# Kernel optimization log

Measured on AMD Instinct MI355X. Metric: run time of the kernel, lower is better.

Reference implementation:

```python
import jax, jax.numpy as jnp
import numpy as np


def setup_inputs() -> dict:
    key = jax.random.key(0)
    kx, kr, kq, kk, kv = jax.random.split(key, 5)
    B, T, N, C = 4, 8, 2048, 128
    w_scale = 1.0 / np.sqrt(C)  # keep logits in a sane range
    return {
        "x": jax.random.normal(kx, (B, T, N, C), dtype=jnp.float32),
        "residual_source": jax.random.normal(kr, (B, N, C), dtype=jnp.float32),
        "Wq": jax.random.normal(kq, (C, C), dtype=jnp.float32) * w_scale,
        "Wk": jax.random.normal(kk, (C, C), dtype=jnp.float32) * w_scale,
        "Wv": jax.random.normal(kv, (C, C), dtype=jnp.float32) * w_scale,
    }


def reference(x, residual_source, Wq, Wk, Wv):
    # x: [B, T, N, C]; residual_source: [B, M, C] (expanded along T in the
    # original via unsqueeze+expand; here we exploit broadcasting instead of
    # materializing the [B, T, M, C] copy -- same math, k/v identical per T).
    q = jnp.einsum("btnc,cd->btnd", x, Wq)               # [B, T, N, D]
    k = jnp.einsum("bmc,cd->bmd", residual_source, Wk)   # [B, M, D]
    v = jnp.einsum("bmc,cd->bmd", residual_source, Wv)   # [B, M, D]
    # Unscaled attention, exactly as in the original (no 1/sqrt(d)).
    affinities = jnp.einsum("btnd,bmd->btnm", q, k)       # [B, T, N, M]
    attn = jax.nn.softmax(affinities, axis=-1)
    residual = jnp.einsum("btnm,bmd->btnd", attn, v)      # [B, T, N, D]
    return x + residual
```

## Files before the change

kernel.cpp:

```cpp
#include <hip/hip_runtime.h>


#define Bn 4
#define Tn 8
#define Nn 2048
#define Cn 128
#define Mn 2048
#define NTILES 32
#define QROWS 128
#define NQT (Nn / QROWS)

typedef __attribute__((ext_vector_type(4))) float f32x4;
typedef __attribute__((ext_vector_type(8))) _Float16 f16x8;
typedef __attribute__((address_space(3))) unsigned char lds_uc;
typedef const __attribute__((address_space(1))) unsigned char glb_uc;

__device__ __forceinline__ unsigned short f2h(float f) {
  _Float16 h = (_Float16)f;
  return __builtin_bit_cast(unsigned short, h);
}
__device__ __forceinline__ f16x8 lds_read8(const unsigned char* base, int row,
                                           int rowBytes, int colByte) {
  int byte = row * rowBytes + (colByte ^ ((row & 7) << 4));
  return *(const f16x8*)(base + byte);
}
__device__ __forceinline__ void gld16(const void* g, void* l) {
  __builtin_amdgcn_global_load_lds((glb_uc*)g, (lds_uc*)l, 16, 0, 0);
}

__global__ __launch_bounds__(256) void proj_kv_kernel(
    const float* __restrict__ rs, const float* __restrict__ Wk,
    const float* __restrict__ Wv, unsigned short* __restrict__ k_ws,
    unsigned short* __restrict__ vt_ws) {
  __shared__ unsigned char smem[48 * 1024];
  unsigned char* rsh = smem;
  unsigned char* wt = smem + 16 * 1024;

  const int bid = blockIdx.x;
  const int b = bid >> 5;
  const int kt = bid & 31;
  const int m0 = kt << 6;
  const int tid = threadIdx.x;
  const int wv = tid >> 6, lane = tid & 63;

  {
    const float4* g = (const float4*)(rs + ((size_t)b * Mn + m0) * Cn);
#pragma unroll
    for (int i = 0; i < 8; ++i) {
      int f = tid + i * 256;
      int row = f >> 5, c4 = f & 31;
      float4 v = g[f];
      int byte = row * 256 + ((c4 * 8) ^ ((row & 7) << 4));
      *(ushort4*)(rsh + byte) =
          make_ushort4(f2h(v.x), f2h(v.y), f2h(v.z), f2h(v.w));
    }
  }

#define STAGE_WT(Wp)                                                          \
  {                                                                           \
    const float4* g = (const float4*)(Wp);                                    \
    _Pragma("unroll") for (int i = 0; i < 16; ++i) {                          \
      int f = tid + i * 256;                                                  \
      int c = f >> 5, d0 = (f & 31) * 4;                                      \
      float4 v = g[f];                                                        \
      float vv[4] = {v.x, v.y, v.z, v.w};                                     \
      _Pragma("unroll") for (int j = 0; j < 4; ++j) {                         \
        int row = d0 + j;                                                     \
        int byte = row * 256 + ((c * 2) ^ ((row & 7) << 4));                  \
        *(unsigned short*)(wt + byte) = f2h(vv[j]);                           \
      }                                                                       \
    }                                                                         \
  }

  STAGE_WT(Wk);
  __syncthreads();

  const int arow = wv * 16 + (lane & 15);
  f16x8 ah[4];
#pragma unroll
  for (int ks = 0; ks < 4; ++ks)
    ah[ks] = lds_read8(rsh, arow, 256, (lane >> 4) * 16 + ks * 64);

  f32x4 acc[8];
#pragma unroll
  for (int df = 0; df < 8; ++df) acc[df] = (f32x4)(0.0f);
#pragma unroll
  for (int ks = 0; ks < 4; ++ks)
#pragma unroll
    for (int df = 0; df < 8; ++df) {
      f16x8 bf = lds_read8(wt, df * 16 + (lane & 15), 256,
                           (lane >> 4) * 16 + ks * 64);
      acc[df] = __builtin_amdgcn_mfma_f32_16x16x32_f16(ah[ks], bf, acc[df], 0, 0, 0);
    }
  {
    unsigned char* kb = (unsigned char*)(k_ws + ((size_t)b * NTILES + kt) * 8192);
#pragma unroll
    for (int df = 0; df < 8; ++df)
#pragma unroll
      for (int r = 0; r < 4; ++r) {
        int row = wv * 16 + (lane >> 4) * 4 + r;
        int dcol = df * 16 + (lane & 15);
        int byte = row * 256 + ((dcol * 2) ^ ((row & 7) << 4));
        *(unsigned short*)(kb + byte) = f2h(acc[df][r]);
      }
  }
  __syncthreads();

  STAGE_WT(Wv);
  __syncthreads();
#pragma unroll
  for (int df = 0; df < 8; ++df) acc[df] = (f32x4)(0.0f);
#pragma unroll
  for (int ks = 0; ks < 4; ++ks)
#pragma unroll
    for (int df = 0; df < 8; ++df) {
      f16x8 bf = lds_read8(wt, df * 16 + (lane & 15), 256,
                           (lane >> 4) * 16 + ks * 64);
      acc[df] = __builtin_amdgcn_mfma_f32_16x16x32_f16(ah[ks], bf, acc[df], 0, 0, 0);
    }
  {
    unsigned char* vb = (unsigned char*)(vt_ws + ((size_t)b * NTILES + kt) * 8192);
#pragma unroll
    for (int df = 0; df < 8; ++df)
#pragma unroll
      for (int r = 0; r < 4; ++r) {
        int row = wv * 16 + (lane >> 4) * 4 + r;
        int dcol = df * 16 + (lane & 15);
        int byte = dcol * 128 + ((row * 2) ^ ((dcol & 7) << 4));
        *(unsigned short*)(vb + byte) = f2h(acc[df][r]);
      }
  }
#undef STAGE_WT
}

__global__ __launch_bounds__(256, 2) void attn_kernel(
    const float* __restrict__ x, const float* __restrict__ Wq,
    const unsigned short* __restrict__ k_ws,
    const unsigned short* __restrict__ vt_ws, float* __restrict__ out) {
  __shared__ unsigned char smem[80 * 1024];

  const int bx = blockIdx.x;
  const int wb = ((bx & 7) << 6) | (bx >> 3);
  const int b = wb >> 7;
  const int t = (wb >> 4) & 7;
  const int n0 = (wb & 15) * QROWS;
  const int tid = threadIdx.x;
  const int wv = tid >> 6, lane = tid & 63;

  const float* xg = x + (((size_t)b * Tn + t) * Nn + n0) * Cn;
  unsigned char* xa = smem;
  unsigned char* wqb = smem + 32 * 1024;
  unsigned char* pb = smem + 64 * 1024 + wv * 4096;

  {
    const float4* g = (const float4*)xg;
#pragma unroll
    for (int i = 0; i < 16; ++i) {
      int f = tid + i * 256;
      int row = f >> 5, c4 = f & 31;
      float4 v = g[f];
      int byte = row * 256 + ((c4 * 8) ^ ((row & 7) << 4));
      *(ushort4*)(xa + byte) =
          make_ushort4(f2h(v.x), f2h(v.y), f2h(v.z), f2h(v.w));
    }
  }
  {
    const float4* g = (const float4*)Wq;
#pragma unroll
    for (int i = 0; i < 16; ++i) {
      int f = tid + i * 256;
      int c = f >> 5, d0 = (f & 31) * 4;
      float4 v = g[f];
      float vv[4] = {v.x, v.y, v.z, v.w};
#pragma unroll
      for (int j = 0; j < 4; ++j) {
        int row = d0 + j;
        int byte = row * 256 + ((c * 2) ^ ((row & 7) << 4));
        *(unsigned short*)(wqb + byte) = f2h(vv[j]);
      }
    }
  }
  __syncthreads();

  f32x4 qacc[2][8];
#pragma unroll
  for (int rb = 0; rb < 2; ++rb)
#pragma unroll
    for (int df = 0; df < 8; ++df) qacc[rb][df] = (f32x4)(0.0f);
  {
    f16x8 xf[2][4];
#pragma unroll
    for (int rb = 0; rb < 2; ++rb)
#pragma unroll
      for (int ks = 0; ks < 4; ++ks)
        xf[rb][ks] = lds_read8(xa, wv * 32 + rb * 16 + (lane & 15), 256,
                               (lane >> 4) * 16 + ks * 64);
#pragma unroll
    for (int ks = 0; ks < 4; ++ks)
#pragma unroll
      for (int df = 0; df < 8; ++df) {
        f16x8 bf = lds_read8(wqb, df * 16 + (lane & 15), 256,
                             (lane >> 4) * 16 + ks * 64);
        qacc[0][df] = __builtin_amdgcn_mfma_f32_16x16x32_f16(xf[0][ks], bf, qacc[0][df], 0, 0, 0);
        qacc[1][df] = __builtin_amdgcn_mfma_f32_16x16x32_f16(xf[1][ks], bf, qacc[1][df], 0, 0, 0);
      }
  }
#pragma unroll
  for (int rb = 0; rb < 2; ++rb)
#pragma unroll
    for (int df = 0; df < 8; ++df)
#pragma unroll
      for (int r = 0; r < 4; ++r) {
        int row = wv * 32 + rb * 16 + (lane >> 4) * 4 + r;
        int col = df * 16 + (lane & 15);
        int byte = row * 256 + ((col * 2) ^ ((row & 7) << 4));
        *(unsigned short*)(xa + byte) = f2h(qacc[rb][df][r]);
      }
  f16x8 qf[2][4];
#pragma unroll
  for (int rb = 0; rb < 2; ++rb)
#pragma unroll
    for (int ks = 0; ks < 4; ++ks)
      qf[rb][ks] = lds_read8(xa, wv * 32 + rb * 16 + (lane & 15), 256,
                             (lane >> 4) * 16 + ks * 64);
  __syncthreads();

  f32x4 o[2][8];
#pragma unroll
  for (int rb = 0; rb < 2; ++rb)
#pragma unroll
    for (int df = 0; df < 8; ++df) o[rb][df] = (f32x4)(0.0f);
  float mrow[2] = {-INFINITY, -INFINITY};
  float lrow[2] = {0.f, 0.f};

  const unsigned char* khg = (const unsigned char*)(k_ws + (size_t)b * NTILES * 8192);
  const unsigned char* vtg = (const unsigned char*)(vt_ws + (size_t)b * NTILES * 8192);

  auto stage = [&](unsigned char* buf, int kt) {
    const unsigned char* kh = khg + (size_t)kt * 16384;
    const unsigned char* vt = vtg + (size_t)kt * 16384;
    int o16 = tid * 16;
#pragma unroll
    for (int h = 0; h < 4; ++h) {
      gld16(kh + o16 + h * 4096, buf + o16 + h * 4096);
      gld16(vt + o16 + h * 4096, buf + 16384 + o16 + h * 4096);
    }
  };

  auto do_tile = [&](unsigned char* buf) {
    unsigned char* kh = buf;
    unsigned char* vt = buf + 16384;
    f32x4 st[2][4];
#pragma unroll
    for (int rb = 0; rb < 2; ++rb)
#pragma unroll
      for (int kvb = 0; kvb < 4; ++kvb) st[rb][kvb] = (f32x4)(0.0f);
    __builtin_amdgcn_s_setprio(1);
#pragma unroll
    for (int ks = 0; ks < 4; ++ks)
#pragma unroll
      for (int kvb = 0; kvb < 4; ++kvb) {
        f16x8 kf = lds_read8(kh, kvb * 16 + (lane & 15), 256,
                             (lane >> 4) * 16 + ks * 64);
        st[0][kvb] = __builtin_amdgcn_mfma_f32_16x16x32_f16(kf, qf[0][ks], st[0][kvb], 0, 0, 0);
        st[1][kvb] = __builtin_amdgcn_mfma_f32_16x16x32_f16(kf, qf[1][ks], st[1][kvb], 0, 0, 0);
      }
    __builtin_amdgcn_s_setprio(0);

#pragma unroll
    for (int rb = 0; rb < 2; ++rb) {
      float tm = st[rb][0][0];
#pragma unroll
      for (int kvb = 0; kvb < 4; ++kvb)
#pragma unroll
        for (int r = 0; r < 4; ++r) tm = fmaxf(tm, st[rb][kvb][r]);
      tm = fmaxf(tm, __shfl_xor(tm, 16));
      tm = fmaxf(tm, __shfl_xor(tm, 32));
      float mn = fmaxf(mrow[rb], tm);
      float scl = __expf(mrow[rb] - mn);
      float rsum = 0.f;
#pragma unroll
      for (int kvb = 0; kvb < 4; ++kvb)
#pragma unroll
        for (int r = 0; r < 4; ++r) {
          float p = __expf(st[rb][kvb][r] - mn);
          st[rb][kvb][r] = p;
          rsum += p;
        }
      rsum += __shfl_xor(rsum, 16);
      rsum += __shfl_xor(rsum, 32);
      lrow[rb] = lrow[rb] * scl + rsum;
      mrow[rb] = mn;
#pragma unroll
      for (int df = 0; df < 8; ++df) o[rb][df] *= scl;
#pragma unroll
      for (int kvb = 0; kvb < 4; ++kvb)
#pragma unroll
        for (int r = 0; r < 4; ++r) {
          int kv = kvb * 16 + (lane >> 4) * 4 + r;
          int byte = (lane & 15) * 128 + ((kv * 2) ^ ((lane & 7) << 4));
          *(unsigned short*)(pb + rb * 2048 + byte) = f2h(st[rb][kvb][r]);
        }
    }
    f16x8 pa[2][2];
#pragma unroll
    for (int rb = 0; rb < 2; ++rb)
#pragma unroll
      for (int ks = 0; ks < 2; ++ks)
        pa[rb][ks] = lds_read8(pb + rb * 2048, lane & 15, 128,
                               (lane >> 4) * 16 + ks * 64);
    __builtin_amdgcn_s_setprio(1);
#pragma unroll
    for (int ks = 0; ks < 2; ++ks)
#pragma unroll
      for (int df = 0; df < 8; ++df) {
        f16x8 vf = lds_read8(vt, df * 16 + (lane & 15), 128,
                             (lane >> 4) * 16 + ks * 64);
        o[0][df] = __builtin_amdgcn_mfma_f32_16x16x32_f16(vf, pa[0][ks], o[0][df], 0, 0, 0);
        o[1][df] = __builtin_amdgcn_mfma_f32_16x16x32_f16(vf, pa[1][ks], o[1][df], 0, 0, 0);
      }
    __builtin_amdgcn_s_setprio(0);
  };

  unsigned char* B0 = smem;
  unsigned char* B1 = smem + 32 * 1024;
  stage(B0, 0);
  __syncthreads();
#pragma unroll 1
  for (int it = 0; it < 16; ++it) {
    int kt = it * 2;
    stage(B1, kt + 1);
    do_tile(B0);
    __syncthreads();
    if (kt + 2 < NTILES) stage(B0, kt + 2);
    do_tile(B1);
    __syncthreads();
  }

  float inv[2] = {1.0f / lrow[0], 1.0f / lrow[1]};
#pragma unroll
  for (int rb = 0; rb < 2; ++rb)
#pragma unroll
    for (int df = 0; df < 8; ++df)
#pragma unroll
      for (int r = 0; r < 4; ++r) {
        int row = wv * 32 + rb * 16 + (lane & 15);
        int d = df * 16 + (lane >> 4) * 4 + r;
        int byte = row * 512 + ((d * 4) ^ ((row & 7) << 4));
        *(float*)(smem + byte) = o[rb][df][r] * inv[rb];
      }
  __syncthreads();
  {
    const float4* xg4 = (const float4*)xg;
    float4* og4 = (float4*)(out + (((size_t)b * Tn + t) * Nn + n0) * Cn);
#pragma unroll
    for (int i = 0; i < 16; ++i) {
      int f = tid + i * 256;
      int row = f >> 5, c4 = f & 31;
      int byte = row * 512 + ((c4 * 16) ^ ((row & 7) << 4));
      f32x4 v = *(const f32x4*)(smem + byte);
      float4 xv = xg4[f];
      og4[f] = make_float4(xv.x + v[0], xv.y + v[1], xv.z + v[2], xv.w + v[3]);
    }
  }
}

extern "C" void kernel_launch(void* const* d_in, const int* in_sizes, int n_in,
                              void* d_out, int out_size, void* d_ws,
                              size_t ws_size, hipStream_t stream) {
  const float* x = (const float*)d_in[0];
  const float* rs = (const float*)d_in[1];
  const float* Wq = (const float*)d_in[2];
  const float* Wk = (const float*)d_in[3];
  const float* Wv = (const float*)d_in[4];
  float* out = (float*)d_out;

  unsigned short* k_ws = (unsigned short*)d_ws;
  unsigned short* vt_ws = k_ws + (size_t)Bn * Mn * Cn;

  proj_kv_kernel<<<Bn * NTILES, 256, 0, stream>>>(rs, Wk, Wv, k_ws, vt_ws);
  attn_kernel<<<Bn * Tn * NQT, 256, 0, stream>>>(x, Wq, k_ws, vt_ws, out);
}
```

Baseline: 122.5 us.

## Load K tiles directly into registers, use exp2 with lazy softmax rescale

K fragments now go straight from global memory into registers, prefetched one tile ahead, instead of being staged through LDS. Only V is double-buffered in shared memory, which shrinks LDS to 64KB and removes the swizzle on the K workspace. The change also folds log2(e) into Q so softmax can use exp2, skips the running-max rescale unless the max grows by more than 8, and defers the row-sum shuffle reduction to the end. P is packed with cvt_pkrtz as well, and block-to-batch mapping changes to improve L2 locality of K/V. The trade-offs are higher register pressure from 16 f16x8 K registers and heavier uncoalesced global loads for K.

```diff
diff --git a/kernel.cpp b/kernel.cpp
--- a/kernel.cpp
+++ b/kernel.cpp
@@ -100,8 +100,7 @@
       for (int r = 0; r < 4; ++r) {
         int row = wv * 16 + (lane >> 4) * 4 + r;
         int dcol = df * 16 + (lane & 15);
-        int byte = row * 256 + ((dcol * 2) ^ ((row & 7) << 4));
-        *(unsigned short*)(kb + byte) = f2h(acc[df][r]);
+        *(unsigned short*)(kb + row * 256 + dcol * 2) = f2h(acc[df][r]);
       }
   }
   __syncthreads();
@@ -137,45 +136,48 @@
     const float* __restrict__ x, const float* __restrict__ Wq,
     const unsigned short* __restrict__ k_ws,
     const unsigned short* __restrict__ vt_ws, float* __restrict__ out) {
-  __shared__ unsigned char smem[80 * 1024];
+  __shared__ unsigned char smem[64 * 1024];
 
   const int bx = blockIdx.x;
-  const int wb = ((bx & 7) << 6) | (bx >> 3);
-  const int b = wb >> 7;
-  const int t = (wb >> 4) & 7;
-  const int n0 = (wb & 15) * QROWS;
+  const int g8 = bx & 7;
+  const int s = bx >> 3;
+  const int b = g8 >> 1;
+  const int i = ((g8 & 1) << 6) | s;
+  const int t = i >> 4;
+  const int n0 = (i & 15) * QROWS;
   const int tid = threadIdx.x;
   const int wv = tid >> 6, lane = tid & 63;
+  const int c = lane & 15, g = lane >> 4;
 
   const float* xg = x + (((size_t)b * Tn + t) * Nn + n0) * Cn;
   unsigned char* xa = smem;
   unsigned char* wqb = smem + 32 * 1024;
-  unsigned char* pb = smem + 64 * 1024 + wv * 4096;
-
-  {
-    const float4* g = (const float4*)xg;
-#pragma unroll
-    for (int i = 0; i < 16; ++i) {
-      int f = tid + i * 256;
+  unsigned char* pb = smem + 32 * 1024 + wv * 4096;
+
+  {
+    const float4* gp = (const float4*)xg;
+#pragma unroll
+    for (int ii = 0; ii < 16; ++ii) {
+      int f = tid + ii * 256;
       int row = f >> 5, c4 = f & 31;
-      float4 v = g[f];
+      float4 v = gp[f];
       int byte = row * 256 + ((c4 * 8) ^ ((row & 7) << 4));
       *(ushort4*)(xa + byte) =
           make_ushort4(f2h(v.x), f2h(v.y), f2h(v.z), f2h(v.w));
     }
   }
   {
-    const float4* g = (const float4*)Wq;
-#pragma unroll
-    for (int i = 0; i < 16; ++i) {
-      int f = tid + i * 256;
-      int c = f >> 5, d0 = (f & 31) * 4;
-      float4 v = g[f];
+    const float4* gp = (const float4*)Wq;
+#pragma unroll
+    for (int ii = 0; ii < 16; ++ii) {
+      int f = tid + ii * 256;
+      int cc = f >> 5, d0 = (f & 31) * 4;
+      float4 v = gp[f];
       float vv[4] = {v.x, v.y, v.z, v.w};
 #pragma unroll
       for (int j = 0; j < 4; ++j) {
         int row = d0 + j;
-        int byte = row * 256 + ((c * 2) ^ ((row & 7) << 4));
+        int byte = row * 256 + ((cc * 2) ^ ((row & 7) << 4));
         *(unsigned short*)(wqb + byte) = f2h(vv[j]);
       }
     }
@@ -193,36 +195,34 @@
     for (int rb = 0; rb < 2; ++rb)
 #pragma unroll
       for (int ks = 0; ks < 4; ++ks)
-        xf[rb][ks] = lds_read8(xa, wv * 32 + rb * 16 + (lane & 15), 256,
-                               (lane >> 4) * 16 + ks * 64);
+        xf[rb][ks] = lds_read8(xa, wv * 32 + rb * 16 + c, 256, g * 16 + ks * 64);
 #pragma unroll
     for (int ks = 0; ks < 4; ++ks)
 #pragma unroll
       for (int df = 0; df < 8; ++df) {
-        f16x8 bf = lds_read8(wqb, df * 16 + (lane & 15), 256,
-                             (lane >> 4) * 16 + ks * 64);
+        f16x8 bf = lds_read8(wqb, df * 16 + c, 256, g * 16 + ks * 64);
         qacc[0][df] = __builtin_amdgcn_mfma_f32_16x16x32_f16(xf[0][ks], bf, qacc[0][df], 0, 0, 0);
         qacc[1][df] = __builtin_amdgcn_mfma_f32_16x16x32_f16(xf[1][ks], bf, qacc[1][df], 0, 0, 0);
       }
   }
+  const float LOG2E = 1.4426950408889634f;
 #pragma unroll
   for (int rb = 0; rb < 2; ++rb)
 #pragma unroll
     for (int df = 0; df < 8; ++df)
 #pragma unroll
       for (int r = 0; r < 4; ++r) {
-        int row = wv * 32 + rb * 16 + (lane >> 4) * 4 + r;
-        int col = df * 16 + (lane & 15);
+        int row = wv * 32 + rb * 16 + g * 4 + r;
+        int col = df * 16 + c;
         int byte = row * 256 + ((col * 2) ^ ((row & 7) << 4));
-        *(unsigned short*)(xa + byte) = f2h(qacc[rb][df][r]);
+        *(unsigned short*)(xa + byte) = f2h(qacc[rb][df][r] * LOG2E);
       }
   f16x8 qf[2][4];
 #pragma unroll
   for (int rb = 0; rb < 2; ++rb)
 #pragma unroll
     for (int ks = 0; ks < 4; ++ks)
-      qf[rb][ks] = lds_read8(xa, wv * 32 + rb * 16 + (lane & 15), 256,
-                             (lane >> 4) * 16 + ks * 64);
+      qf[rb][ks] = lds_read8(xa, wv * 32 + rb * 16 + c, 256, g * 16 + ks * 64);
   __syncthreads();
 
   f32x4 o[2][8];
@@ -235,21 +235,37 @@
 
   const unsigned char* khg = (const unsigned char*)(k_ws + (size_t)b * NTILES * 8192);
   const unsigned char* vtg = (const unsigned char*)(vt_ws + (size_t)b * NTILES * 8192);
-
+  const int klane = c * 256 + g * 16;
+
+  auto kload = [&](f16x8* kreg, int kt) {
+    const unsigned char* kb = khg + (size_t)kt * 16384 + klane;
+#pragma unroll
+    for (int ks = 0; ks < 4; ++ks)
+#pragma unroll
+      for (int kvb = 0; kvb < 4; ++kvb)
+        kreg[ks * 4 + kvb] = *(const f16x8*)(kb + kvb * 4096 + ks * 64);
+  };
   auto stage = [&](unsigned char* buf, int kt) {
-    const unsigned char* kh = khg + (size_t)kt * 16384;
     const unsigned char* vt = vtg + (size_t)kt * 16384;
     int o16 = tid * 16;
 #pragma unroll
-    for (int h = 0; h < 4; ++h) {
-      gld16(kh + o16 + h * 4096, buf + o16 + h * 4096);
-      gld16(vt + o16 + h * 4096, buf + 16384 + o16 + h * 4096);
-    }
+    for (int h = 0; h < 4; ++h)
+      gld16(vt + o16 + h * 4096, buf + o16 + h * 4096);
   };
 
-  auto do_tile = [&](unsigned char* buf) {
-    unsigned char* kh = buf;
-    unsigned char* vt = buf + 16384;
+  unsigned char* B0 = smem;
+  unsigned char* B1 = smem + 16 * 1024;
+
+  f16x8 kreg[16];
+  stage(B0, 0);
+  kload(kreg, 0);
+  __syncthreads();
+
+#pragma unroll 1
+  for (int it = 0; it < NTILES; ++it) {
+    unsigned char* curv = (it & 1) ? B1 : B0;
+    unsigned char* altv = (it & 1) ? B0 : B1;
+
     f32x4 st[2][4];
 #pragma unroll
     for (int rb = 0; rb < 2; ++rb)
@@ -260,12 +276,16 @@
     for (int ks = 0; ks < 4; ++ks)
 #pragma unroll
       for (int kvb = 0; kvb < 4; ++kvb) {
-        f16x8 kf = lds_read8(kh, kvb * 16 + (lane & 15), 256,
-                             (lane >> 4) * 16 + ks * 64);
+        f16x8 kf = kreg[ks * 4 + kvb];
         st[0][kvb] = __builtin_amdgcn_mfma_f32_16x16x32_f16(kf, qf[0][ks], st[0][kvb], 0, 0, 0);
         st[1][kvb] = __builtin_amdgcn_mfma_f32_16x16x32_f16(kf, qf[1][ks], st[1][kvb], 0, 0, 0);
       }
     __builtin_amdgcn_s_setprio(0);
+
+    if (it + 1 < NTILES) {
+      kload(kreg, it + 1);
+      stage(altv, it + 1);
+    }
 
 #pragma unroll
     for (int rb = 0; rb < 2; ++rb) {
@@ -276,67 +296,62 @@
         for (int r = 0; r < 4; ++r) tm = fmaxf(tm, st[rb][kvb][r]);
       tm = fmaxf(tm, __shfl_xor(tm, 16));
       tm = fmaxf(tm, __shfl_xor(tm, 32));
-      float mn = fmaxf(mrow[rb], tm);
-      float scl = __expf(mrow[rb] - mn);
-      float rsum = 0.f;
-#pragma unroll
-      for (int kvb = 0; kvb < 4; ++kvb)
+      float mn = mrow[rb];
+      if (__any(tm > mn + 8.f)) {
+        float newm = fmaxf(mn, tm);
+        float scl = exp2f(mn - newm);
+#pragma unroll
+        for (int df = 0; df < 8; ++df) o[rb][df] *= scl;
+        lrow[rb] *= scl;
+        mrow[rb] = newm;
+        mn = newm;
+      }
+      float ps = 0.f;
+#pragma unroll
+      for (int kvb = 0; kvb < 4; ++kvb) {
 #pragma unroll
         for (int r = 0; r < 4; ++r) {
-          float p = __expf(st[rb][kvb][r] - mn);
+          float p = exp2f(st[rb][kvb][r] - mn);
           st[rb][kvb][r] = p;
-          rsum += p;
+          ps += p;
         }
-      rsum += __shfl_xor(rsum, 16);
-      rsum += __shfl_xor(rsum, 32);
-      lrow[rb] = lrow[rb] * scl + rsum;
-      mrow[rb] = mn;
-#pragma unroll
-      for (int df = 0; df < 8; ++df) o[rb][df] *= scl;
-#pragma unroll
-      for (int kvb = 0; kvb < 4; ++kvb)
-#pragma unroll
-        for (int r = 0; r < 4; ++r) {
-          int kv = kvb * 16 + (lane >> 4) * 4 + r;
-          int byte = (lane & 15) * 128 + ((kv * 2) ^ ((lane & 7) << 4));
-          *(unsigned short*)(pb + rb * 2048 + byte) = f2h(st[rb][kvb][r]);
+#pragma unroll
+        for (int h = 0; h < 2; ++h) {
+          auto pk = __builtin_amdgcn_cvt_pkrtz(st[rb][kvb][2 * h],
+                                               st[rb][kvb][2 * h + 1]);
+          int kv2 = kvb * 32 + g * 8 + h * 4;
+          int byte = c * 128 + (kv2 ^ ((c & 7) << 4));
+          *(unsigned int*)(pb + rb * 2048 + byte) =
+              __builtin_bit_cast(unsigned int, pk);
         }
-    }
+      }
+      lrow[rb] += ps;
+    }
+
     f16x8 pa[2][2];
 #pragma unroll
     for (int rb = 0; rb < 2; ++rb)
 #pragma unroll
       for (int ks = 0; ks < 2; ++ks)
-        pa[rb][ks] = lds_read8(pb + rb * 2048, lane & 15, 128,
-                               (lane >> 4) * 16 + ks * 64);
+        pa[rb][ks] = lds_read8(pb + rb * 2048, c, 128, g * 16 + ks * 64);
     __builtin_amdgcn_s_setprio(1);
 #pragma unroll
     for (int ks = 0; ks < 2; ++ks)
 #pragma unroll
       for (int df = 0; df < 8; ++df) {
-        f16x8 vf = lds_read8(vt, df * 16 + (lane & 15), 128,
-                             (lane >> 4) * 16 + ks * 64);
+        f16x8 vf = lds_read8(curv, df * 16 + c, 128, g * 16 + ks * 64);
         o[0][df] = __builtin_amdgcn_mfma_f32_16x16x32_f16(vf, pa[0][ks], o[0][df], 0, 0, 0);
         o[1][df] = __builtin_amdgcn_mfma_f32_16x16x32_f16(vf, pa[1][ks], o[1][df], 0, 0, 0);
       }
     __builtin_amdgcn_s_setprio(0);
-  };
-
-  unsigned char* B0 = smem;
-  unsigned char* B1 = smem + 32 * 1024;
-  stage(B0, 0);
-  __syncthreads();
-#pragma unroll 1
-  for (int it = 0; it < 16; ++it) {
-    int kt = it * 2;
-    stage(B1, kt + 1);
-    do_tile(B0);
     __syncthreads();
-    if (kt + 2 < NTILES) stage(B0, kt + 2);
-    do_tile(B1);
-    __syncthreads();
-  }
-
+  }
+
+#pragma unroll
+  for (int rb = 0; rb < 2; ++rb) {
+    lrow[rb] += __shfl_xor(lrow[rb], 16);
+    lrow[rb] += __shfl_xor(lrow[rb], 32);
+  }
   float inv[2] = {1.0f / lrow[0], 1.0f / lrow[1]};
 #pragma unroll
   for (int rb = 0; rb < 2; ++rb)
@@ -344,8 +359,8 @@
     for (int df = 0; df < 8; ++df)
 #pragma unroll
       for (int r = 0; r < 4; ++r) {
-        int row = wv * 32 + rb * 16 + (lane & 15);
-        int d = df * 16 + (lane >> 4) * 4 + r;
+        int row = wv * 32 + rb * 16 + c;
+        int d = df * 16 + g * 4 + r;
         int byte = row * 512 + ((d * 4) ^ ((row & 7) << 4));
         *(float*)(smem + byte) = o[rb][df][r] * inv[rb];
       }
@@ -354,8 +369,8 @@
     const float4* xg4 = (const float4*)xg;
     float4* og4 = (float4*)(out + (((size_t)b * Tn + t) * Nn + n0) * Cn);
 #pragma unroll
-    for (int i = 0; i < 16; ++i) {
-      int f = tid + i * 256;
+    for (int ii = 0; ii < 16; ++ii) {
+      int f = tid + ii * 256;
       int row = f >> 5, c4 = f & 31;
       int byte = row * 512 + ((c4 * 16) ^ ((row & 7) << 4));
       f32x4 v = *(const f32x4*)(smem + byte);
```

Result: slower. 179.4 us (+46.4%).
